# Optimization experiments

Hardware: AMD Instinct MI355X
Metric: run time of the kernel (lower is better)

## Reference

```python
import jax, jax.numpy as jnp
import numpy as np

K = 3; STRIDE = 1; PAD = 1
IN_C = 256; OUT_C = 512
SPAN = K * K * IN_C        # 2304, im2col row count
M = 3                      # ALSH augmentation dims
TABLE_SIZE = 8             # hash buckets
R = 2.5                    # LSH bin width


def setup_inputs() -> dict:
    key = jax.random.key(0)
    k1, k2, k3, k4 = jax.random.split(key, 4)
    stdv = 1.0 / np.sqrt(SPAN)
    inp = jax.random.normal(k1, (16, IN_C, 56, 56), dtype=jnp.float32)
    kernels = jax.random.uniform(k2, (OUT_C, SPAN), minval=-stdv, maxval=stdv,
                                 dtype=jnp.float32)
    a_hash = jax.random.normal(k3, (SPAN + M,), dtype=jnp.float32)
    b_hash = jax.random.uniform(k4, (1,), dtype=jnp.float32) * R
    return {"input": inp, "kernels": kernels, "a_hash": a_hash,
            "b_hash": b_hash, "mode": 1}


def _P(x, m):
    # ALSH P-augmentation: append ||x||^(2^i), i=1..m, per row. x: [O, SPAN]
    n = jnp.linalg.norm(x, axis=1, keepdims=True)
    ext = jnp.concatenate([n ** (2 ** (i + 1)) for i in range(m)], axis=1)
    return jnp.concatenate([x, ext], axis=1)  # [O, SPAN+M]


def _bucket(vals, b, r, ts):
    # floor((v+b)/r) ; fmod ts ; abs  (matches torch fmod-then-abs semantics)
    idx = jnp.floor((vals + b) / r).astype(jnp.int32)
    return jnp.abs(jnp.fmod(idx, ts))


def _im2col_matr(x):
    # [N, C, H, W] -> [SPAN, N*H2*W2]
    n = x.shape[0]
    h2 = (x.shape[2] - K + 2 * PAD) // STRIDE + 1
    w2 = (x.shape[3] - K + 2 * PAD) // STRIDE + 1
    patches = jax.lax.conv_general_dilated_patches(
        x, (K, K), (STRIDE, STRIDE), [(PAD, PAD), (PAD, PAD)])  # [N, SPAN, H2, W2]
    return patches.reshape(n, SPAN, h2 * w2).transpose(1, 0, 2).reshape(SPAN, -1), h2, w2


def reference(input, kernels, a_hash, b_hash, mode):
    n = input.shape[0]
    patch_matr, h2, w2 = _im2col_matr(input)  # [SPAN, L]

    # ---- build ALSH table: bucket of each kernel row ----
    kvals = _P(kernels, M) @ a_hash           # [OUT_C]
    kbuck = _bucket(kvals, b_hash[0], R, TABLE_SIZE)

    # ---- vote: hash every unit-normalized patch column, take modal bucket ----
    unit = patch_matr / jnp.linalg.norm(patch_matr, axis=0, keepdims=True)
    q_ext = jnp.full((M, unit.shape[1]), 0.5, dtype=unit.dtype)
    votes = a_hash @ jnp.concatenate([unit, q_ext], axis=0)  # [L]
    vbuck = _bucket(votes, b_hash[0], R, TABLE_SIZE)
    counts = jnp.bincount(vbuck, length=TABLE_SIZE)
    bucket = int(jnp.argmax(counts))

    # ---- gather active kernel rows for that bucket (data-dependent) ----
    rows = np.sort(np.where(np.asarray(kbuck) == bucket)[0])
    if rows.size != 0:
        active = kernels[jnp.asarray(rows)]          # [oc, SPAN]
        out = active @ patch_matr                    # [oc, L]
        if mode:
            out = out / (float(rows.size) / OUT_C)
        oc = int(rows.size)
    else:
        out = kernels @ patch_matr
        oc = OUT_C

    out = out.reshape(oc, n, h2 * w2).transpose(1, 0, 2).reshape(n, oc, h2, w2)
    return (out, jnp.asarray(rows, dtype=jnp.int32))
```

## Files before the change

### kernel.cpp

```cpp
#include <hip/hip_runtime.h>
#include <math.h>

#define N_    16
#define C_    256
#define H_    56
#define W_    56
#define HW_   3136
#define NPIX  50176
#define OUTC  512
#define SPAN_ 2304
#define BLKPX 256
#define HBYTES 24576

typedef unsigned short u16;
typedef unsigned int   u32;
typedef __attribute__((ext_vector_type(8))) short bf16x8;
typedef __attribute__((ext_vector_type(8))) unsigned short u16x8;
typedef __attribute__((ext_vector_type(4))) float f32x4;
typedef __attribute__((ext_vector_type(4))) unsigned short u16x4;

__device__ __forceinline__ u16 f2bf(float v) {
    u32 x = __float_as_uint(v);
    u32 r = (x + 0x7fffu + ((x >> 16) & 1u)) >> 16;
    return (u16)r;
}

__device__ __forceinline__ int bucketf(float v, float b) {
    int idx = (int)floorf((v + b) / 2.5f);
    int r = idx % 8;
    return r < 0 ? -r : r;
}

__global__ __launch_bounds__(256) void prep_fused(const float* __restrict__ x,
                                                  const float* __restrict__ ah,
                                                  const float* __restrict__ bh,
                                                  const float* __restrict__ kern,
                                                  u16* __restrict__ xp,
                                                  float* __restrict__ g,
                                                  float* __restrict__ s2,
                                                  int* __restrict__ kbuck) {
    int kb = blockIdx.x - (NPIX / 64);
    int t = threadIdx.x;
    if (kb >= 0) {
        int oc_l = t >> 2, part = t & 3;
        int oc = kb * 64 + oc_l;
        const float* kr = kern + (size_t)oc * SPAN_ + part * 576;
        const float* ap = ah + part * 576;
        float dot = 0.f, ss = 0.f;
        for (int i = 0; i < 144; ++i) {
            float4 kv = *(const float4*)(kr + i * 4);
            float4 av = *(const float4*)(ap + i * 4);
            dot += kv.x * av.x + kv.y * av.y + kv.z * av.z + kv.w * av.w;
            ss  += kv.x * kv.x + kv.y * kv.y + kv.z * kv.z + kv.w * kv.w;
        }
        dot += __shfl_xor(dot, 1); dot += __shfl_xor(dot, 2);
        ss  += __shfl_xor(ss, 1);  ss  += __shfl_xor(ss, 2);
        if (part == 0) {
            float n2 = ss;
            float n4 = n2 * n2;
            float n8 = n4 * n4;
            float v = dot + n2 * ah[SPAN_] + n4 * ah[SPAN_ + 1] +
                      n8 * ah[SPAN_ + 2];
            kbuck[oc] = bucketf(v, bh[0]);
        }
        return;
    }

    __shared__ float aL[SPAN_];
    __shared__ u16 tl[64][68];
    __shared__ float red[4][64][10];
    for (int j = t; j < SPAN_; j += 256) aL[j] = ah[j];

    int px0 = blockIdx.x * 64;
    int img = px0 / HW_;
    int hw0 = px0 - img * HW_;
    int px_l = t & 63;
    int cq   = t >> 6;
    float pg[9];
#pragma unroll
    for (int kk = 0; kk < 9; ++kk) pg[kk] = 0.f;
    float ps = 0.f;
    __syncthreads();

    for (int cb0 = 0; cb0 < 4; ++cb0) {
        int c0 = cb0 * 64;
#pragma unroll
        for (int rep = 0; rep < 16; ++rep) {
            int c_l = rep * 4 + cq;
            float v = x[((size_t)(img * C_ + c0 + c_l)) * HW_ + hw0 + px_l];
            tl[px_l][c_l] = f2bf(v);
            const float* ac = &aL[(c0 + c_l) * 9];
#pragma unroll
            for (int kk = 0; kk < 9; ++kk) pg[kk] += ac[kk] * v;
            ps += v * v;
        }
        __syncthreads();
        int c4  = t & 15;
        int pxs = t >> 4;
#pragma unroll
        for (int rep = 0; rep < 4; ++rep) {
            int pl = rep * 16 + pxs;
            u16x4 v4 = *(const u16x4*)(&tl[pl][c4 * 4]);
            *(u16x4*)(&xp[((size_t)(px0 + pl)) * C_ + c0 + c4 * 4]) = v4;
        }
        __syncthreads();
    }

#pragma unroll
    for (int kk = 0; kk < 9; ++kk) red[cq][px_l][kk] = pg[kk];
    red[cq][px_l][9] = ps;
    __syncthreads();
    for (int it = t; it < 640; it += 256) {
        int pl = it / 10;
        int j  = it - pl * 10;
        float s = red[0][pl][j] + red[1][pl][j] + red[2][pl][j] + red[3][pl][j];
        int q = px0 + pl;
        if (j < 9) g[(size_t)j * NPIX + q] = s;
        else       s2[q] = s;
    }
}

__global__ __launch_bounds__(256) void vote_kernel(const float* __restrict__ g,
                                                   const float* __restrict__ s2,
                                                   const float* __restrict__ ah,
                                                   const float* __restrict__ bh,
                                                   int* __restrict__ counts) {
    __shared__ int hist[8];
    if (threadIdx.x < 8) hist[threadIdx.x] = 0;
    __syncthreads();
    int q = blockIdx.x * 256 + threadIdx.x;
    int n = q / HW_;
    int p = q - n * HW_;
    int h = p / W_;
    int w = p - h * W_;
    float dot = 0.f, ss = 0.f;
#pragma unroll
    for (int kk = 0; kk < 9; ++kk) {
        int dh = kk / 3 - 1, dw = kk % 3 - 1;
        int hh = h + dh, ww = w + dw;
        if (hh >= 0 && hh < H_ && ww >= 0 && ww < W_) {
            int idx = n * HW_ + hh * W_ + ww;
            dot += g[(size_t)kk * NPIX + idx];
            ss  += s2[idx];
        }
    }
    float qext = 0.5f * (ah[SPAN_] + ah[SPAN_ + 1] + ah[SPAN_ + 2]);
    float v = dot / sqrtf(ss) + qext;
    int b = bucketf(v, bh[0]);
    atomicAdd(&hist[b], 1);
    __syncthreads();
    if (threadIdx.x < 8) atomicAdd(&counts[threadIdx.x], hist[threadIdx.x]);
}

__global__ __launch_bounds__(256) void prep_w(const float* __restrict__ kern,
                                              const int* __restrict__ kbuck,
                                              const int* __restrict__ counts,
                                              const int* __restrict__ mode,
                                              float* __restrict__ out,
                                              u16* __restrict__ wfrag,
                                              int nfB, int oc_total) {
    __shared__ int sc[256];
    __shared__ int rowsL[512];
    int t = threadIdx.x;
    int best = 0, bc = counts[0];
#pragma unroll
    for (int i = 1; i < 8; ++i) {
        int c = counts[i];
        if (c > bc) { bc = c; best = i; }
    }
    int f0 = (kbuck[t] == best) ? 1 : 0;
    int f1 = (kbuck[t + 256] == best) ? 1 : 0;
    sc[t] = f0 | (f1 << 16);
    __syncthreads();
    for (int off = 1; off < 256; off <<= 1) {
        int add = (t >= off) ? sc[t - off] : 0;
        __syncthreads();
        sc[t] += add;
        __syncthreads();
    }
    int tot = sc[255];
    int t0  = tot & 0xffff;
    int cnt = t0 + (tot >> 16);
    int pos0 = (sc[t] & 0xffff) - f0;
    int pos1 = t0 + (sc[t] >> 16) - f1;
    rowsL[t] = 0; rowsL[t + 256] = 0;
    __syncthreads();
    if (cnt == 0) { rowsL[t] = t; rowsL[t + 256] = t + 256; }
    else {
        if (f0) rowsL[pos0] = t;
        if (f1) rowsL[pos1] = t + 256;
    }
    __syncthreads();
    int ocEff = (cnt == 0) ? OUTC : cnt;
    float scale = (mode[0] && cnt > 0) ? 512.0f / (float)cnt : 1.0f;

    if (blockIdx.x == 0) {
        float* rout = out + (size_t)N_ * oc_total * HW_;
        int nw = ocEff < oc_total ? ocEff : oc_total;
        if (cnt == 0) {
            if (t < nw) rout[t] = (float)t;
            if (t + 256 < nw) rout[t + 256] = (float)(t + 256);
        } else {
            if (f0 && pos0 < nw) rout[pos0] = (float)t;
            if (f1 && pos1 < nw) rout[pos1] = (float)(t + 256);
        }
    }

    int e = blockIdx.x * 256 + t;
    int lane = e & 63;
    int t2 = e >> 6;
    int g = t2 % nfB;
    int s = t2 / nfB;
    int kk = s >> 3;
    int cb = s & 7;
    int q = lane >> 4;
    int mcol = lane & 15;
    int oc_i = g * 16 + mcol;
    bool valid = oc_i < ocEff;
    int row = valid ? rowsL[oc_i] : 0;
    const float* kr = kern + (size_t)row * SPAN_;
    u16 w8[8];
#pragma unroll
    for (int j = 0; j < 8; ++j) {
        int c = cb * 32 + q * 8 + j;
        float v = valid ? kr[c * 9 + kk] * scale : 0.f;
        w8[j] = f2bf(v);
    }
    u16* dst = wfrag + ((size_t)((s * nfB + g) * 64 + lane)) * 8;
#pragma unroll
    for (int j = 0; j < 8; ++j) dst[j] = w8[j];
}

__global__ __launch_bounds__(256, 2) void conv_mfma(const u16* __restrict__ xp,
                                                    const u16* __restrict__ wfrag,
                                                    float* __restrict__ out,
                                                    int nfB, int oc_total, int nby) {
    __shared__ char halo[2 * HBYTES];

    int flat = blockIdx.x;
    int bx, by;
    int full = 192 * nby;
    if (flat < full) {
        int gsz = 8 * nby;
        int gi = flat / gsz;
        int tr = flat - gi * gsz;
        by = tr >> 3;
        bx = gi * 8 + (tr & 7);
    } else {
        int tr = flat - full;
        by = tr >> 2;
        bx = 192 + (tr & 3);
    }

    const int t = threadIdx.x;
    const int lane = t & 63;
    const int wv = t >> 6;
    const int pb = bx * BLKPX;
    const int fb = by * 3;
    const int lane15 = lane & 15;
    const int laneq  = lane >> 4;

    u32 valMask[4];
    int aB[4][3];
#pragma unroll
    for (int f = 0; f < 4; ++f) {
        int p = pb + wv * 64 + f * 16 + lane15;
        int img = p / HW_;
        int rp = p - img * HW_;
        int h = rp / W_;
        int w = rp - h * W_;
        u32 m = 0;
#pragma unroll
        for (int kk = 0; kk < 9; ++kk) {
            int dh = kk / 3 - 1, dw = kk % 3 - 1;
            int hh = h + dh, ww = w + dw;
            if (hh >= 0 && hh < H_ && ww >= 0 && ww < W_) m |= (1u << kk);
        }
        valMask[f] = m;
#pragma unroll
        for (int j = 0; j < 3; ++j) {
            int sn = 57 + wv * 64 + f * 16 + lane15 + (j - 1);
            aB[f][j] = sn * 64 + ((laneq ^ ((sn >> 1) & 3)) << 4) - 3584;
        }
    }

    f32x4 acc[4][3];
#pragma unroll
    for (int f = 0; f < 4; ++f)
#pragma unroll
        for (int gg = 0; gg < 3; ++gg) acc[f][gg] = (f32x4){0.f, 0.f, 0.f, 0.f};
    const bf16x8 zf = {0, 0, 0, 0, 0, 0, 0, 0};

    const char* xpb = (const char*)xp;
    const int q4 = (((t & 3) ^ ((t >> 3) & 3)) << 4);
    int gpx[6];
#pragma unroll
    for (int r = 0; r < 6; ++r) {
        int p = pb - 57 + r * 64 + (t >> 2);
        gpx[r] = p < 0 ? 0 : (p >= NPIX ? NPIX - 1 : p);
    }

#pragma unroll
    for (int r = 0; r < 6; ++r)
        __builtin_amdgcn_global_load_lds(
            (const __attribute__((address_space(1))) unsigned int*)
                (xpb + (size_t)gpx[r] * 512 + q4),
            (__attribute__((address_space(3))) unsigned int*)&halo[r * 4096 + t * 16],
            16, 0, 0);

    const size_t cbStride = (size_t)nfB * 512;
    const size_t kkStride = cbStride * 8;
    const u16* wl = wfrag + (size_t)fb * 512 + (size_t)lane * 8;
    bf16x8 bW[3], bWn[3];
#define LOADB(dst, cb_, kk_) do {                                               \
    const u16* _wp = wl + (size_t)(kk_) * kkStride + (size_t)(cb_) * cbStride;  \
    _Pragma("unroll")                                                           \
    for (int _g = 0; _g < 3; ++_g)                                              \
        dst[_g] = *(const bf16x8*)(_wp + (size_t)_g * 512);                     \
} while (0)

    LOADB(bW, 0, 0);

#pragma unroll
    for (int cb = 0; cb < 8; ++cb) {
        __syncthreads();

        if (cb < 7) {
            const int nb = ((cb + 1) & 1) * HBYTES;
#pragma unroll
            for (int r = 0; r < 6; ++r)
                __builtin_amdgcn_global_load_lds(
                    (const __attribute__((address_space(1))) unsigned int*)
                        (xpb + (size_t)gpx[r] * 512 + (cb + 1) * 64 + q4),
                    (__attribute__((address_space(3))) unsigned int*)
                        &halo[nb + r * 4096 + t * 16],
                    16, 0, 0);
        }

#pragma unroll
        for (int kk = 0; kk < 9; ++kk) {
            if (kk < 8)       LOADB(bWn, cb, kk + 1);
            else if (cb < 7)  LOADB(bWn, cb + 1, 0);

            const int dh = kk / 3 - 1;
            const int j  = kk % 3;
            const int IMM = (cb & 1) * HBYTES + (dh + 1) * 3584;
            bf16x8 aX[4];
#pragma unroll
            for (int f = 0; f < 4; ++f) {
                bf16x8 a = *(const bf16x8*)&halo[aB[f][j] + IMM];
                aX[f] = ((valMask[f] >> kk) & 1) ? a : zf;
            }
#pragma unroll
            for (int gg = 0; gg < 3; ++gg)
#pragma unroll
                for (int f = 0; f < 4; ++f)
                    acc[f][gg] = __builtin_amdgcn_mfma_f32_16x16x32_bf16(
                        aX[f], bW[gg], acc[f][gg], 0, 0, 0);
            if (kk < 8 || cb < 7) {
#pragma unroll
                for (int gg = 0; gg < 3; ++gg) bW[gg] = bWn[gg];
            }
        }
    }
#undef LOADB

#pragma unroll
    for (int f = 0; f < 4; ++f) {
        int p0 = pb + wv * 64 + f * 16 + laneq * 4;
        int img0 = p0 / HW_;
        int hw0 = p0 - img0 * HW_;
#pragma unroll
        for (int gg = 0; gg < 3; ++gg) {
            int oc = (fb + gg) * 16 + lane15;
            if (oc < oc_total) {
                float* op = out + ((size_t)img0 * oc_total + oc) * HW_ + hw0;
                *(f32x4*)op = acc[f][gg];
            }
        }
    }
}

extern "C" void kernel_launch(void* const* d_in, const int* in_sizes, int n_in,
                              void* d_out, int out_size, void* d_ws, size_t ws_size,
                              hipStream_t stream) {
    const float* x    = (const float*)d_in[0];
    const float* kern = (const float*)d_in[1];
    const float* ah   = (const float*)d_in[2];
    const float* bh   = (const float*)d_in[3];
    const int*   mode = (const int*)d_in[4];
    float* out = (float*)d_out;

    int oc_total = (out_size % (N_ * HW_ + 1) == 0) ? out_size / (N_ * HW_ + 1)
                                                    : OUTC;
    int nfTot = (oc_total + 15) / 16;
    int nby   = (nfTot + 2) / 3;
    int nfB   = nby * 3;

    u16*   xp     = (u16*)d_ws;
    u16*   wfrag  = xp + (size_t)NPIX * C_;
    float* g      = (float*)(wfrag + (size_t)72 * 36 * 64 * 8);
    float* s2     = g + (size_t)9 * NPIX;
    int*   counts = (int*)(s2 + NPIX);
    int*   kbuck  = counts + 8;

    hipMemsetAsync(counts, 0, 8 * sizeof(int), stream);

    prep_fused<<<NPIX / 64 + 8, 256, 0, stream>>>(x, ah, bh, kern, xp, g, s2,
                                                  kbuck);
    vote_kernel<<<NPIX / 256, 256, 0, stream>>>(g, s2, ah, bh, counts);
    prep_w<<<18 * nfB, 256, 0, stream>>>(kern, kbuck, counts, mode, out, wfrag,
                                         nfB, oc_total);
    conv_mfma<<<(NPIX / BLKPX) * nby, 256, 0, stream>>>(xp, wfrag, out, nfB,
                                                        oc_total, nby);
}
```

Before: 106.6 us.

## Restructure prep kernel: one pixel per thread, prefetched channel loads, fold memset

```diff
diff --git a/kernel.cpp b/kernel.cpp
--- a/kernel.cpp
+++ b/kernel.cpp
@@ -11,6 +11,8 @@
 #define SPAN_ 2304
 #define BLKPX 256
 #define HBYTES 24576
+#define PXB   128
+#define NPB   (NPIX / PXB)
 
 typedef unsigned short u16;
 typedef unsigned int   u32;
@@ -31,30 +33,32 @@
     return r < 0 ? -r : r;
 }
 
-__global__ __launch_bounds__(256) void prep_fused(const float* __restrict__ x,
-                                                  const float* __restrict__ ah,
-                                                  const float* __restrict__ bh,
-                                                  const float* __restrict__ kern,
-                                                  u16* __restrict__ xp,
-                                                  float* __restrict__ g,
-                                                  float* __restrict__ s2,
-                                                  int* __restrict__ kbuck) {
-    int kb = blockIdx.x - (NPIX / 64);
+__global__ __launch_bounds__(128) void prep2(const float* __restrict__ x,
+                                             const float* __restrict__ ah,
+                                             const float* __restrict__ bh,
+                                             const float* __restrict__ kern,
+                                             u16* __restrict__ xp,
+                                             float* __restrict__ g,
+                                             float* __restrict__ s2,
+                                             int* __restrict__ kbuck,
+                                             int* __restrict__ counts) {
+    int kb = blockIdx.x - NPB;
     int t = threadIdx.x;
     if (kb >= 0) {
-        int oc_l = t >> 2, part = t & 3;
+        if (kb == 0 && t < 8) counts[t] = 0;
+        int oc_l = t >> 1, part = t & 1;
         int oc = kb * 64 + oc_l;
-        const float* kr = kern + (size_t)oc * SPAN_ + part * 576;
-        const float* ap = ah + part * 576;
+        const float* kr = kern + (size_t)oc * SPAN_ + part * 1152;
+        const float* ap = ah + part * 1152;
         float dot = 0.f, ss = 0.f;
-        for (int i = 0; i < 144; ++i) {
+        for (int i = 0; i < 288; ++i) {
             float4 kv = *(const float4*)(kr + i * 4);
             float4 av = *(const float4*)(ap + i * 4);
             dot += kv.x * av.x + kv.y * av.y + kv.z * av.z + kv.w * av.w;
             ss  += kv.x * kv.x + kv.y * kv.y + kv.z * kv.z + kv.w * kv.w;
         }
-        dot += __shfl_xor(dot, 1); dot += __shfl_xor(dot, 2);
-        ss  += __shfl_xor(ss, 1);  ss  += __shfl_xor(ss, 2);
+        dot += __shfl_xor(dot, 1);
+        ss  += __shfl_xor(ss, 1);
         if (part == 0) {
             float n2 = ss;
             float n4 = n2 * n2;
@@ -67,57 +71,61 @@
     }
 
     __shared__ float aL[SPAN_];
-    __shared__ u16 tl[64][68];
-    __shared__ float red[4][64][10];
-    for (int j = t; j < SPAN_; j += 256) aL[j] = ah[j];
-
-    int px0 = blockIdx.x * 64;
-    int img = px0 / HW_;
-    int hw0 = px0 - img * HW_;
-    int px_l = t & 63;
-    int cq   = t >> 6;
+    __shared__ u16 tl[PXB][68];
+    for (int j = t; j < SPAN_; j += 128) aL[j] = ah[j];
+
+    const int px = blockIdx.x * PXB + t;
+    const int img = px / HW_;
+    const size_t xbase = (size_t)img * C_ * HW_ + (px - img * HW_);
+
     float pg[9];
 #pragma unroll
     for (int kk = 0; kk < 9; ++kk) pg[kk] = 0.f;
     float ps = 0.f;
     __syncthreads();
 
-    for (int cb0 = 0; cb0 < 4; ++cb0) {
-        int c0 = cb0 * 64;
-#pragma unroll
-        for (int rep = 0; rep < 16; ++rep) {
-            int c_l = rep * 4 + cq;
-            float v = x[((size_t)(img * C_ + c0 + c_l)) * HW_ + hw0 + px_l];
-            tl[px_l][c_l] = f2bf(v);
-            const float* ac = &aL[(c0 + c_l) * 9];
-#pragma unroll
-            for (int kk = 0; kk < 9; ++kk) pg[kk] += ac[kk] * v;
-            ps += v * v;
+    for (int ph = 0; ph < 4; ++ph) {
+        float R[16], Rn[16];
+#pragma unroll
+        for (int i = 0; i < 16; ++i)
+            R[i] = x[xbase + (size_t)(ph * 64 + i) * HW_];
+#pragma unroll
+        for (int sub = 0; sub < 4; ++sub) {
+            if (sub < 3) {
+#pragma unroll
+                for (int i = 0; i < 16; ++i)
+                    Rn[i] = x[xbase + (size_t)(ph * 64 + (sub + 1) * 16 + i) * HW_];
+            }
+#pragma unroll
+            for (int i = 0; i < 16; ++i) {
+                int c = ph * 64 + sub * 16 + i;
+                float v = R[i];
+                const float* ac = &aL[c * 9];
+#pragma unroll
+                for (int kk = 0; kk < 9; ++kk) pg[kk] += ac[kk] * v;
+                ps += v * v;
+                tl[t][sub * 16 + i] = f2bf(v);
+            }
+            if (sub < 3) {
+#pragma unroll
+                for (int i = 0; i < 16; ++i) R[i] = Rn[i];
+            }
         }
         __syncthreads();
-        int c4  = t & 15;
-        int pxs = t >> 4;
-#pragma unroll
-        for (int rep = 0; rep < 4; ++rep) {
-            int pl = rep * 16 + pxs;
-            u16x4 v4 = *(const u16x4*)(&tl[pl][c4 * 4]);
-            *(u16x4*)(&xp[((size_t)(px0 + pl)) * C_ + c0 + c4 * 4]) = v4;
+        const int oct = t & 7;
+#pragma unroll
+        for (int pass = 0; pass < 8; ++pass) {
+            int pxl = pass * 16 + (t >> 3);
+            u16x8 v8 = *(const u16x8*)&tl[pxl][oct * 8];
+            *(u16x8*)&xp[((size_t)(blockIdx.x * PXB + pxl)) * C_ +
+                         ph * 64 + oct * 8] = v8;
         }
         __syncthreads();
     }
 
 #pragma unroll
-    for (int kk = 0; kk < 9; ++kk) red[cq][px_l][kk] = pg[kk];
-    red[cq][px_l][9] = ps;
-    __syncthreads();
-    for (int it = t; it < 640; it += 256) {
-        int pl = it / 10;
-        int j  = it - pl * 10;
-        float s = red[0][pl][j] + red[1][pl][j] + red[2][pl][j] + red[3][pl][j];
-        int q = px0 + pl;
-        if (j < 9) g[(size_t)j * NPIX + q] = s;
-        else       s2[q] = s;
-    }
+    for (int kk = 0; kk < 9; ++kk) g[(size_t)kk * NPIX + px] = pg[kk];
+    s2[px] = ps;
 }
 
 __global__ __launch_bounds__(256) void vote_kernel(const float* __restrict__ g,
@@ -404,10 +412,8 @@
     int*   counts = (int*)(s2 + NPIX);
     int*   kbuck  = counts + 8;
 
-    hipMemsetAsync(counts, 0, 8 * sizeof(int), stream);
-
-    prep_fused<<<NPIX / 64 + 8, 256, 0, stream>>>(x, ah, bh, kern, xp, g, s2,
-                                                  kbuck);
+    prep2<<<NPB + 8, 128, 0, stream>>>(x, ah, bh, kern, xp, g, s2, kbuck,
+                                       counts);
     vote_kernel<<<NPIX / 256, 256, 0, stream>>>(g, s2, ah, bh, counts);
     prep_w<<<18 * nfB, 256, 0, stream>>>(kern, kbuck, counts, mode, out, wfrag,
                                          nfB, oc_total);
```

New measurement: 93.47 us. 1.14x faster.
